# Optimization experiments

Measured on AMD Instinct MI355X. Metric: run time of the kernel, lower is better.

Reference implementation:

```python
import jax, jax.numpy as jnp
import numpy as np

N_QUAT = 4
VERONESE_DIM = 10
OUT_FEATURES = 132

# static index sets matching torch.triu_indices(4, 4)
_rows, _cols = np.triu_indices(N_QUAT)          # 10 upper-tri entries
_mask = _rows != _cols
TRIU_ROWS = jnp.asarray(_rows)
TRIU_COLS = jnp.asarray(_cols)
SYM_ROWS = jnp.asarray(_cols[_mask])            # mirrored lower-tri
SYM_COLS = jnp.asarray(_rows[_mask])
SYM_Z_IDX = jnp.asarray(np.nonzero(_mask)[0])


def setup_inputs() -> dict:
    key = jax.random.key(0)
    k_z, k_w1, k_w2 = jax.random.split(key, 3)
    B, D_IN, D_HID, D_OUT_NN = 65536, 256, 1024, 128
    z = jax.random.normal(k_z, (B, D_IN), dtype=jnp.float32)
    W1 = jax.random.normal(k_w1, (D_IN, D_HID), dtype=jnp.float32) * 0.02
    b1 = jnp.zeros((D_HID,), dtype=jnp.float32)
    W2 = jax.random.normal(k_w2, (D_HID, D_OUT_NN), dtype=jnp.float32) * 0.02
    b2 = jnp.zeros((D_OUT_NN,), dtype=jnp.float32)
    return {"z": z, "W1": W1, "b1": b1, "W2": W2, "b2": b2}


def _recover_quat(z_v):
    # z_v: (B, 10) -> symmetric (B, 4, 4) -> top eigenvector -> (B, 4)
    B = z_v.shape[0]
    M = jnp.zeros((B, N_QUAT, N_QUAT), dtype=z_v.dtype)
    M = M.at[:, TRIU_ROWS, TRIU_COLS].set(z_v)
    M = M.at[:, SYM_ROWS, SYM_COLS].set(z_v[:, SYM_Z_IDX])
    _, vecs = jnp.linalg.eigh(M)          # eigenvalues ascending
    q = vecs[:, :, -1]                    # eigenvector of largest eigenvalue
    sign = jnp.sign(q[:, 0:1] + 1e-9)
    return q * sign


def reference(z, W1, b1, W2, b2):
    orig_shape = z.shape
    zf = z.reshape(-1, orig_shape[-1])           # (B, in_features)
    q_pred = _recover_quat(zf[:, :VERONESE_DIM])  # (B, 4)
    h = jax.nn.relu(zf @ W1 + b1)
    others = h @ W2 + b2                          # (B, 128)
    B = zf.shape[0]
    out = jnp.zeros((B, OUT_FEATURES), dtype=zf.dtype)
    out = out.at[:, :N_QUAT].set(q_pred)          # quat_indices = [0,1,2,3]
    out = out.at[:, N_QUAT:].set(others)          # non_quat = [4..131]
    return out.reshape(*orig_shape[:-1], OUT_FEATURES)
```

## Files before the change

kernel.cpp:

```cpp
#include <hip/hip_runtime.h>


typedef short s16x8 __attribute__((ext_vector_type(8)));
typedef float f32x4 __attribute__((ext_vector_type(4)));
typedef float f32x16 __attribute__((ext_vector_type(16)));
typedef unsigned char u8;

__device__ __forceinline__ f32x16 mfma32(s16x8 a, s16x8 b, f32x16 c) {
    return __builtin_amdgcn_mfma_f32_32x32x16_bf16(a, b, c, 0, 0, 0);
}

__device__ __forceinline__ short f2bf(float f) {
    unsigned int u = __float_as_uint(f);
    u = (u + 0x7fffu + ((u >> 16) & 1u)) >> 16;
    return (short)u;
}

__device__ __forceinline__ unsigned cvt_pk(float lo, float hi) {
    unsigned r;
    asm("v_cvt_pk_bf16_f32 %0, %1, %2" : "=v"(r) : "v"(lo), "v"(hi));
    return r;
}

__device__ __forceinline__ void pl32swap(unsigned& a, unsigned& b) {
    asm("v_permlane32_swap_b32 %0, %1" : "+v"(a), "+v"(b));
}

__device__ __forceinline__ void gload_lds16(const void* g, void* l) {
    __builtin_amdgcn_global_load_lds(
        (const __attribute__((address_space(1))) unsigned int*)g,
        (__attribute__((address_space(3))) unsigned int*)l, 16, 0, 0);
}

__global__ __launch_bounds__(256) void prep_weights(
    const float* __restrict__ W1, const float* __restrict__ W2,
    uint4* __restrict__ w1t, uint4* __restrict__ w2t)
{
    int tid = blockIdx.x * 256 + threadIdx.x;
    int hl = (tid >> 5) & 1, r32 = tid & 31;
    union { short b[8]; uint4 v; } pk;
    if (tid < 32768) {
        int s  = (tid >> 6) & 15;
        int ct = (tid >> 10) & 1;
        int c  = tid >> 11;
        int k0 = s * 16 + hl * 8;
        int n1 = c * 64 + ct * 32 + r32;
        #pragma unroll
        for (int j = 0; j < 8; ++j)
            pk.b[j] = f2bf(W1[(k0 + j) * 1024 + n1]);
        w1t[tid] = pk.v;
    } else {
        int g  = tid - 32768;
        int nt = (g >> 6) & 3;
        int K  = g >> 8;
        int k0 = K * 16 + hl * 8;
        int n2 = nt * 32 + r32;
        #pragma unroll
        for (int j = 0; j < 8; ++j)
            pk.b[j] = f2bf(W2[(k0 + j) * 128 + n2]);
        w2t[g] = pk.v;
    }
}

__global__ __launch_bounds__(256, 2) void fused_all(
    const float* __restrict__ z, const float* __restrict__ b1,
    const float* __restrict__ b2, const uint4* __restrict__ w1t,
    const uint4* __restrict__ w2t, float* __restrict__ out)
{
    __shared__ __align__(16) u8 lds[69632];

    const int t    = threadIdx.x;
    const int lane = t & 63;
    const int w    = t >> 6;
    const int hl   = lane >> 5;
    const int r32  = lane & 31;
    const int bm0  = blockIdx.x * 128;
    const int rowbase = bm0 + w * 32;

    #pragma unroll
    for (int i = 0; i < 8; ++i) {
        int f = i * 256 + t;
        gload_lds16(w1t + f, lds + f * 16);
    }
    gload_lds16(b1 + t * 4, lds + 65536 + t * 16);

    if (lane < 32) {
        int row = rowbase + lane;
        const float* zr = z + (size_t)row * 256;
        float4 v0 = *(const float4*)(zr);
        float4 v1 = *(const float4*)(zr + 4);
        float2 v2 = *(const float2*)(zr + 8);

        float A[4][4] = {{v0.x, v0.y, v0.z, v0.w},
                         {v0.y, v1.x, v1.y, v1.z},
                         {v0.z, v1.y, v1.w, v2.x},
                         {v0.w, v1.z, v2.x, v2.y}};
        float V[4][4] = {{1.f, 0.f, 0.f, 0.f},
                         {0.f, 1.f, 0.f, 0.f},
                         {0.f, 0.f, 1.f, 0.f},
                         {0.f, 0.f, 0.f, 1.f}};

#define ROT(p, qq) do {                                                   \
        float apq  = A[p][qq];                                            \
        float tau  = (A[qq][qq] - A[p][p]) *                              \
                     __builtin_amdgcn_rcpf(2.0f * apq);                   \
        float tt   = __builtin_amdgcn_rcpf(                               \
                        fabsf(tau) +                                      \
                        __builtin_amdgcn_sqrtf(fmaf(tau, tau, 1.0f)));    \
        tt = copysignf(tt, tau);                                          \
        tt = (fabsf(apq) > 1e-20f) ? tt : 0.0f;                           \
        float cth = __builtin_amdgcn_rsqf(fmaf(tt, tt, 1.0f));            \
        float sth = tt * cth;                                             \
        _Pragma("unroll")                                                 \
        for (int k = 0; k < 4; ++k) {                                     \
            float akp = A[k][p], akq = A[k][qq];                          \
            A[k][p]  = cth * akp - sth * akq;                             \
            A[k][qq] = sth * akp + cth * akq;                             \
        }                                                                 \
        _Pragma("unroll")                                                 \
        for (int k = 0; k < 4; ++k) {                                     \
            float apk = A[p][k], aqk = A[qq][k];                          \
            A[p][k]  = cth * apk - sth * aqk;                             \
            A[qq][k] = sth * apk + cth * aqk;                             \
        }                                                                 \
        _Pragma("unroll")                                                 \
        for (int k = 0; k < 4; ++k) {                                     \
            float vkp = V[k][p], vkq = V[k][qq];                          \
            V[k][p]  = cth * vkp - sth * vkq;                             \
            V[k][qq] = sth * vkp + cth * vkq;                             \
        }                                                                 \
    } while (0)

        #pragma unroll 1
        for (int sweep = 0; sweep < 6; ++sweep) {
            ROT(0, 1); ROT(0, 2); ROT(0, 3); ROT(1, 2); ROT(1, 3); ROT(2, 3);
        }
#undef ROT

        float bv = A[0][0];
        float q0 = V[0][0], q1 = V[1][0], q2 = V[2][0], q3 = V[3][0];
        #pragma unroll
        for (int k = 1; k < 4; ++k) {
            bool better = A[k][k] > bv;
            bv = better ? A[k][k] : bv;
            q0 = better ? V[0][k] : q0;
            q1 = better ? V[1][k] : q1;
            q2 = better ? V[2][k] : q2;
            q3 = better ? V[3][k] : q3;
        }
        float sgn = (q0 + 1e-9f) >= 0.0f ? 1.0f : -1.0f;
        *(float4*)(out + (size_t)row * 132) =
            make_float4(sgn * q0, sgn * q1, sgn * q2, sgn * q3);
    }

    s16x8 zf[16];
    {
        const float* zp = z + (size_t)(rowbase + r32) * 256 + hl * 8;
        #pragma unroll
        for (int s = 0; s < 16; ++s) {
            float4 a0 = *(const float4*)(zp + s * 16);
            float4 a1 = *(const float4*)(zp + s * 16 + 4);
            union { unsigned u[4]; s16x8 v; } pk;
            pk.u[0] = cvt_pk(a0.x, a0.y);
            pk.u[1] = cvt_pk(a0.z, a0.w);
            pk.u[2] = cvt_pk(a1.x, a1.y);
            pk.u[3] = cvt_pk(a1.z, a1.w);
            zf[s] = pk.v;
        }
    }

    const f32x16 zero16 = {0.f,0.f,0.f,0.f, 0.f,0.f,0.f,0.f,
                           0.f,0.f,0.f,0.f, 0.f,0.f,0.f,0.f};
    f32x16 acc2[4];
    #pragma unroll
    for (int nt = 0; nt < 4; ++nt) acc2[nt] = zero16;

    __syncthreads();

    const u8* const aW0  = lds + lane * 16;
    const u8* const aW1  = lds + 32768 + lane * 16;
    const u8* const blsp = lds + 65536 + hl * 16;
    const s16x8* const w2b = (const s16x8*)w2t + lane;

    u8* const s1b0 = lds;
    u8* const s1b1 = lds + 32768;

    auto chunk = [&](int c, const u8* a, u8* s1dst) {
        const s16x8* w2c = w2b + c * 1024;
        s16x8 w2f[4][4];
        #pragma unroll
        for (int ks = 0; ks < 2; ++ks)
            #pragma unroll
            for (int nt = 0; nt < 4; ++nt)
                w2f[ks][nt] = w2c[(ks * 4 + nt) * 64];

        if (c < 15) {
            const uint4* s1 = w1t + (c + 1) * 2048;
            #pragma unroll
            for (int i = 0; i < 8; ++i) {
                int f = i * 256 + t;
                gload_lds16(s1 + f, s1dst + f * 16);
            }
        }

        const u8* bb = blsp + c * 256;
        s16x8 hf[4];

        auto tile = [&](int ct) {
            __builtin_amdgcn_s_setprio(1);
            f32x16 d = zero16;
            #pragma unroll
            for (int s = 0; s < 16; ++s) {
                s16x8 afr = *(const s16x8*)(a + (ct * 16 + s) * 1024);
                d = mfma32(afr, zf[s], d);
            }
            __builtin_amdgcn_s_setprio(0);
            unsigned Plo[4], Phi[4];
            #pragma unroll
            for (int g = 0; g < 4; ++g) {
                f32x4 bv = *(const f32x4*)(bb + ct * 128 + g * 32);
                Plo[g] = cvt_pk(fmaxf(d[4*g+0] + bv[0], 0.f),
                                fmaxf(d[4*g+1] + bv[1], 0.f));
                Phi[g] = cvt_pk(fmaxf(d[4*g+2] + bv[2], 0.f),
                                fmaxf(d[4*g+3] + bv[3], 0.f));
            }
            #pragma unroll
            for (int f = 0; f < 2; ++f) {
                unsigned a0 = Plo[2*f], b0 = Plo[2*f+1];
                unsigned a1 = Phi[2*f], b1 = Phi[2*f+1];
                pl32swap(a0, b0);
                pl32swap(a1, b1);
                union { unsigned u[4]; s16x8 v; } fr;
                fr.u[0] = a0; fr.u[1] = a1; fr.u[2] = b0; fr.u[3] = b1;
                hf[ct * 2 + f] = fr.v;
            }
        };

        tile(0);
        #pragma unroll
        for (int ks = 2; ks < 4; ++ks)
            #pragma unroll
            for (int nt = 0; nt < 4; ++nt)
                w2f[ks][nt] = w2c[(ks * 4 + nt) * 64];
        __builtin_amdgcn_s_setprio(1);
        #pragma unroll
        for (int ks = 0; ks < 2; ++ks)
            #pragma unroll
            for (int nt = 0; nt < 4; ++nt)
                acc2[nt] = mfma32(hf[ks], w2f[ks][nt], acc2[nt]);
        __builtin_amdgcn_s_setprio(0);

        tile(1);
        __builtin_amdgcn_s_setprio(1);
        #pragma unroll
        for (int ks = 2; ks < 4; ++ks)
            #pragma unroll
            for (int nt = 0; nt < 4; ++nt)
                acc2[nt] = mfma32(hf[ks], w2f[ks][nt], acc2[nt]);
        __builtin_amdgcn_s_setprio(0);

        __syncthreads();
    };

    #pragma unroll 1
    for (int cc = 0; cc < 8; ++cc) {
        chunk(2 * cc,     aW0, s1b1);
        chunk(2 * cc + 1, aW1, s1b0);
    }

    #pragma unroll
    for (int nt = 0; nt < 4; ++nt) {
        const float b2v = b2[nt * 32 + r32];
        #pragma unroll
        for (int r = 0; r < 16; ++r) {
            int m = w * 32 + (r & 3) + 8 * (r >> 2) + 4 * hl;
            out[(size_t)(bm0 + m) * 132 + 4 + nt * 32 + r32] =
                acc2[nt][r] + b2v;
        }
    }
}

extern "C" void kernel_launch(void* const* d_in, const int* in_sizes, int n_in,
                              void* d_out, int out_size, void* d_ws, size_t ws_size,
                              hipStream_t stream) {
    const float* z  = (const float*)d_in[0];
    const float* W1 = (const float*)d_in[1];
    const float* b1 = (const float*)d_in[2];
    const float* W2 = (const float*)d_in[3];
    const float* b2 = (const float*)d_in[4];
    float* out = (float*)d_out;

    uint4* w1t = (uint4*)d_ws;
    uint4* w2t = (uint4*)((char*)d_ws + 512 * 1024);

    hipLaunchKernelGGL(prep_weights, dim3(192), dim3(256), 0, stream,
                       W1, W2, w1t, w2t);
    hipLaunchKernelGGL(fused_all, dim3(512), dim3(256), 0, stream,
                       z, b1, b2, (const uint4*)w1t, (const uint4*)w2t, out);
}
```

Before: 73.13 us.

## Software-pipeline GEMM2 of previous chunk into GEMM1 MFMA loop

Restructures the fused MLP chunk loop so the second GEMM for chunk c-1 runs interleaved with the first GEMM of chunk c. The two 32-wide GEMM1 tiles are computed together, and the bias/ReLU/bf16 packing is deferred to the end of the chunk. A prologue chunk and an epilogue GEMM2 are added. The aim is to hide the dependency stall between GEMM1 output and GEMM2 input, at the cost of more live registers (hfp, two accumulators).

```diff
diff --git a/kernel.cpp b/kernel.cpp
--- a/kernel.cpp
+++ b/kernel.cpp
@@ -185,14 +185,40 @@
     u8* const s1b0 = lds;
     u8* const s1b1 = lds + 32768;
 
-    auto chunk = [&](int c, const u8* a, u8* s1dst) {
-        const s16x8* w2c = w2b + c * 1024;
+    s16x8 hfp[4];
+
+    auto pack = [&](const f32x16& d, const u8* bb, int ct, s16x8* hfo) {
+        unsigned Plo[4], Phi[4];
+        #pragma unroll
+        for (int g = 0; g < 4; ++g) {
+            f32x4 bv = *(const f32x4*)(bb + ct * 128 + g * 32);
+            Plo[g] = cvt_pk(fmaxf(d[4*g+0] + bv[0], 0.f),
+                            fmaxf(d[4*g+1] + bv[1], 0.f));
+            Phi[g] = cvt_pk(fmaxf(d[4*g+2] + bv[2], 0.f),
+                            fmaxf(d[4*g+3] + bv[3], 0.f));
+        }
+        #pragma unroll
+        for (int f = 0; f < 2; ++f) {
+            unsigned a0 = Plo[2*f], b0 = Plo[2*f+1];
+            unsigned a1 = Phi[2*f], b1 = Phi[2*f+1];
+            pl32swap(a0, b0);
+            pl32swap(a1, b1);
+            union { unsigned u[4]; s16x8 v; } fr;
+            fr.u[0] = a0; fr.u[1] = a1; fr.u[2] = b0; fr.u[3] = b1;
+            hfo[f] = fr.v;
+        }
+    };
+
+    auto chunk = [&](int c, const u8* a, u8* s1dst, bool DO_G2) {
         s16x8 w2f[4][4];
-        #pragma unroll
-        for (int ks = 0; ks < 2; ++ks)
+        const s16x8* w2c = w2b + (c - 1) * 1024;
+        if (DO_G2) {
             #pragma unroll
-            for (int nt = 0; nt < 4; ++nt)
-                w2f[ks][nt] = w2c[(ks * 4 + nt) * 64];
+            for (int ks = 0; ks < 2; ++ks)
+                #pragma unroll
+                for (int nt = 0; nt < 4; ++nt)
+                    w2f[ks][nt] = w2c[(ks * 4 + nt) * 64];
+        }
 
         if (c < 15) {
             const uint4* s1 = w1t + (c + 1) * 2048;
@@ -204,68 +230,54 @@
         }
 
         const u8* bb = blsp + c * 256;
-        s16x8 hf[4];
-
-        auto tile = [&](int ct) {
-            __builtin_amdgcn_s_setprio(1);
-            f32x16 d = zero16;
-            #pragma unroll
-            for (int s = 0; s < 16; ++s) {
-                s16x8 afr = *(const s16x8*)(a + (ct * 16 + s) * 1024);
-                d = mfma32(afr, zf[s], d);
+
+        __builtin_amdgcn_s_setprio(1);
+        f32x16 d0 = zero16, d1 = zero16;
+        #pragma unroll
+        for (int s = 0; s < 16; ++s) {
+            s16x8 a0 = *(const s16x8*)(a + s * 1024);
+            s16x8 a1 = *(const s16x8*)(a + (16 + s) * 1024);
+            d0 = mfma32(a0, zf[s], d0);
+            d1 = mfma32(a1, zf[s], d1);
+            if (DO_G2 && s == 4) {
+                #pragma unroll
+                for (int ks = 2; ks < 4; ++ks)
+                    #pragma unroll
+                    for (int nt = 0; nt < 4; ++nt)
+                        w2f[ks][nt] = w2c[(ks * 4 + nt) * 64];
             }
-            __builtin_amdgcn_s_setprio(0);
-            unsigned Plo[4], Phi[4];
-            #pragma unroll
-            for (int g = 0; g < 4; ++g) {
-                f32x4 bv = *(const f32x4*)(bb + ct * 128 + g * 32);
-                Plo[g] = cvt_pk(fmaxf(d[4*g+0] + bv[0], 0.f),
-                                fmaxf(d[4*g+1] + bv[1], 0.f));
-                Phi[g] = cvt_pk(fmaxf(d[4*g+2] + bv[2], 0.f),
-                                fmaxf(d[4*g+3] + bv[3], 0.f));
+            if (DO_G2 && s >= 8) {
+                int i = s - 8, ks = i >> 1, nt0 = (i & 1) * 2;
+                acc2[nt0]     = mfma32(hfp[ks], w2f[ks][nt0],     acc2[nt0]);
+                acc2[nt0 + 1] = mfma32(hfp[ks], w2f[ks][nt0 + 1], acc2[nt0 + 1]);
             }
-            #pragma unroll
-            for (int f = 0; f < 2; ++f) {
-                unsigned a0 = Plo[2*f], b0 = Plo[2*f+1];
-                unsigned a1 = Phi[2*f], b1 = Phi[2*f+1];
-                pl32swap(a0, b0);
-                pl32swap(a1, b1);
-                union { unsigned u[4]; s16x8 v; } fr;
-                fr.u[0] = a0; fr.u[1] = a1; fr.u[2] = b0; fr.u[3] = b1;
-                hf[ct * 2 + f] = fr.v;
-            }
-        };
-
-        tile(0);
-        #pragma unroll
-        for (int ks = 2; ks < 4; ++ks)
-            #pragma unroll
-            for (int nt = 0; nt < 4; ++nt)
-                w2f[ks][nt] = w2c[(ks * 4 + nt) * 64];
-        __builtin_amdgcn_s_setprio(1);
-        #pragma unroll
-        for (int ks = 0; ks < 2; ++ks)
-            #pragma unroll
-            for (int nt = 0; nt < 4; ++nt)
-                acc2[nt] = mfma32(hf[ks], w2f[ks][nt], acc2[nt]);
+        }
         __builtin_amdgcn_s_setprio(0);
 
-        tile(1);
-        __builtin_amdgcn_s_setprio(1);
-        #pragma unroll
-        for (int ks = 2; ks < 4; ++ks)
-            #pragma unroll
-            for (int nt = 0; nt < 4; ++nt)
-                acc2[nt] = mfma32(hf[ks], w2f[ks][nt], acc2[nt]);
-        __builtin_amdgcn_s_setprio(0);
+        pack(d0, bb, 0, hfp);
+        pack(d1, bb, 1, hfp + 2);
 
         __syncthreads();
     };
 
+    chunk(0, aW0, s1b1, false);
     #pragma unroll 1
-    for (int cc = 0; cc < 8; ++cc) {
-        chunk(2 * cc,     aW0, s1b1);
-        chunk(2 * cc + 1, aW1, s1b0);
+    for (int cc = 0; cc < 7; ++cc) {
+        chunk(2 * cc + 1, aW1, s1b0, true);
+        chunk(2 * cc + 2, aW0, s1b1, true);
+    }
+    chunk(15, aW1, s1b0, true);
+
+    {
+        const s16x8* w2c = w2b + 15 * 1024;
+        #pragma unroll
+        for (int ks = 0; ks < 4; ++ks) {
+            #pragma unroll
+            for (int nt = 0; nt < 4; ++nt) {
+                s16x8 bfr = w2c[(ks * 4 + nt) * 64];
+                acc2[nt] = mfma32(hfp[ks], bfr, acc2[nt]);
+            }
+        }
     }
 
     #pragma unroll
```

After: 76.25 us. +4.3%, slower.

## Drop LDS staging of W1; single-wave blocks read weights directly from global

Applied to the files above, without the earlier changes.

Replaces the 4-wave block that cooperatively double-buffers W1 chunks and b1 in LDS with 1-wave blocks (2048 of them). Each wave now loads its W1 fragments, b1 and W2 directly from global memory via L2/cache. This removes the LDS staging, the barriers and the 68KB LDS footprint that limited occupancy. In exchange every wave fetches the full weight matrix itself, which raises global/L2 traffic fourfold and puts load latency directly in front of the MFMAs.

```diff
diff --git a/kernel.cpp b/kernel.cpp
--- a/kernel.cpp
+++ b/kernel.cpp
@@ -24,12 +24,6 @@
 
 __device__ __forceinline__ void pl32swap(unsigned& a, unsigned& b) {
     asm("v_permlane32_swap_b32 %0, %1" : "+v"(a), "+v"(b));
-}
-
-__device__ __forceinline__ void gload_lds16(const void* g, void* l) {
-    __builtin_amdgcn_global_load_lds(
-        (const __attribute__((address_space(1))) unsigned int*)g,
-        (__attribute__((address_space(3))) unsigned int*)l, 16, 0, 0);
 }
 
 __global__ __launch_bounds__(256) void prep_weights(
@@ -62,27 +56,15 @@
     }
 }
 
-__global__ __launch_bounds__(256, 2) void fused_all(
+__global__ __launch_bounds__(64, 2) void fused_all(
     const float* __restrict__ z, const float* __restrict__ b1,
     const float* __restrict__ b2, const uint4* __restrict__ w1t,
     const uint4* __restrict__ w2t, float* __restrict__ out)
 {
-    __shared__ __align__(16) u8 lds[69632];
-
-    const int t    = threadIdx.x;
-    const int lane = t & 63;
-    const int w    = t >> 6;
+    const int lane = threadIdx.x & 63;
     const int hl   = lane >> 5;
     const int r32  = lane & 31;
-    const int bm0  = blockIdx.x * 128;
-    const int rowbase = bm0 + w * 32;
-
-    #pragma unroll
-    for (int i = 0; i < 8; ++i) {
-        int f = i * 256 + t;
-        gload_lds16(w1t + f, lds + f * 16);
-    }
-    gload_lds16(b1 + t * 4, lds + 65536 + t * 16);
+    const int rowbase = blockIdx.x * 32;
 
     if (lane < 32) {
         int row = rowbase + lane;
@@ -175,97 +157,55 @@
     #pragma unroll
     for (int nt = 0; nt < 4; ++nt) acc2[nt] = zero16;
 
-    __syncthreads();
-
-    const u8* const aW0  = lds + lane * 16;
-    const u8* const aW1  = lds + 32768 + lane * 16;
-    const u8* const blsp = lds + 65536 + hl * 16;
+    const s16x8* const w1b = (const s16x8*)w1t + lane;
     const s16x8* const w2b = (const s16x8*)w2t + lane;
-
-    u8* const s1b0 = lds;
-    u8* const s1b1 = lds + 32768;
-
-    auto chunk = [&](int c, const u8* a, u8* s1dst) {
+    const float* const bbp = b1 + hl * 4;
+
+    s16x8 hf[4];
+
+    auto pack = [&](const f32x16& d, int c, int ct, s16x8* hfo) {
+        unsigned Plo[4], Phi[4];
+        #pragma unroll
+        for (int g = 0; g < 4; ++g) {
+            f32x4 bv = *(const f32x4*)(bbp + c * 64 + ct * 32 + g * 8);
+            Plo[g] = cvt_pk(fmaxf(d[4*g+0] + bv[0], 0.f),
+                            fmaxf(d[4*g+1] + bv[1], 0.f));
+            Phi[g] = cvt_pk(fmaxf(d[4*g+2] + bv[2], 0.f),
+                            fmaxf(d[4*g+3] + bv[3], 0.f));
+        }
+        #pragma unroll
+        for (int f = 0; f < 2; ++f) {
+            unsigned a0 = Plo[2*f], b0 = Plo[2*f+1];
+            unsigned a1 = Phi[2*f], b1_ = Phi[2*f+1];
+            pl32swap(a0, b0);
+            pl32swap(a1, b1_);
+            union { unsigned u[4]; s16x8 v; } fr;
+            fr.u[0] = a0; fr.u[1] = a1; fr.u[2] = b0; fr.u[3] = b1_;
+            hfo[f] = fr.v;
+        }
+    };
+
+    #pragma unroll 2
+    for (int c = 0; c < 16; ++c) {
+        const s16x8* w1c = w1b + c * 2048;
+        #pragma unroll
+        for (int ct = 0; ct < 2; ++ct) {
+            f32x16 d = zero16;
+            __builtin_amdgcn_s_setprio(1);
+            #pragma unroll
+            for (int s = 0; s < 16; ++s)
+                d = mfma32(w1c[(ct * 16 + s) * 64], zf[s], d);
+            __builtin_amdgcn_s_setprio(0);
+            pack(d, c, ct, hf + 2 * ct);
+        }
         const s16x8* w2c = w2b + c * 1024;
-        s16x8 w2f[4][4];
-        #pragma unroll
-        for (int ks = 0; ks < 2; ++ks)
+        __builtin_amdgcn_s_setprio(1);
+        #pragma unroll
+        for (int ks = 0; ks < 4; ++ks)
             #pragma unroll
             for (int nt = 0; nt < 4; ++nt)
-                w2f[ks][nt] = w2c[(ks * 4 + nt) * 64];
-
-        if (c < 15) {
-            const uint4* s1 = w1t + (c + 1) * 2048;
-            #pragma unroll
-            for (int i = 0; i < 8; ++i) {
-                int f = i * 256 + t;
-                gload_lds16(s1 + f, s1dst + f * 16);
-            }
-        }
-
-        const u8* bb = blsp + c * 256;
-        s16x8 hf[4];
-
-        auto tile = [&](int ct) {
-            __builtin_amdgcn_s_setprio(1);
-            f32x16 d = zero16;
-            #pragma unroll
-            for (int s = 0; s < 16; ++s) {
-                s16x8 afr = *(const s16x8*)(a + (ct * 16 + s) * 1024);
-                d = mfma32(afr, zf[s], d);
-            }
-            __builtin_amdgcn_s_setprio(0);
-            unsigned Plo[4], Phi[4];
-            #pragma unroll
-            for (int g = 0; g < 4; ++g) {
-                f32x4 bv = *(const f32x4*)(bb + ct * 128 + g * 32);
-                Plo[g] = cvt_pk(fmaxf(d[4*g+0] + bv[0], 0.f),
-                                fmaxf(d[4*g+1] + bv[1], 0.f));
-                Phi[g] = cvt_pk(fmaxf(d[4*g+2] + bv[2], 0.f),
-                                fmaxf(d[4*g+3] + bv[3], 0.f));
-            }
-            #pragma unroll
-            for (int f = 0; f < 2; ++f) {
-                unsigned a0 = Plo[2*f], b0 = Plo[2*f+1];
-                unsigned a1 = Phi[2*f], b1 = Phi[2*f+1];
-                pl32swap(a0, b0);
-                pl32swap(a1, b1);
-                union { unsigned u[4]; s16x8 v; } fr;
-                fr.u[0] = a0; fr.u[1] = a1; fr.u[2] = b0; fr.u[3] = b1;
-                hf[ct * 2 + f] = fr.v;
-            }
-        };
-
-        tile(0);
-        #pragma unroll
-        for (int ks = 2; ks < 4; ++ks)
-            #pragma unroll
-            for (int nt = 0; nt < 4; ++nt)
-                w2f[ks][nt] = w2c[(ks * 4 + nt) * 64];
-        __builtin_amdgcn_s_setprio(1);
-        #pragma unroll
-        for (int ks = 0; ks < 2; ++ks)
-            #pragma unroll
-            for (int nt = 0; nt < 4; ++nt)
-                acc2[nt] = mfma32(hf[ks], w2f[ks][nt], acc2[nt]);
+                acc2[nt] = mfma32(hf[ks], w2c[(ks * 4 + nt) * 64], acc2[nt]);
         __builtin_amdgcn_s_setprio(0);
-
-        tile(1);
-        __builtin_amdgcn_s_setprio(1);
-        #pragma unroll
-        for (int ks = 2; ks < 4; ++ks)
-            #pragma unroll
-            for (int nt = 0; nt < 4; ++nt)
-                acc2[nt] = mfma32(hf[ks], w2f[ks][nt], acc2[nt]);
-        __builtin_amdgcn_s_setprio(0);
-
-        __syncthreads();
-    };
-
-    #pragma unroll 1
-    for (int cc = 0; cc < 8; ++cc) {
-        chunk(2 * cc,     aW0, s1b1);
-        chunk(2 * cc + 1, aW1, s1b0);
     }
 
     #pragma unroll
@@ -273,8 +213,8 @@
         const float b2v = b2[nt * 32 + r32];
         #pragma unroll
         for (int r = 0; r < 16; ++r) {
-            int m = w * 32 + (r & 3) + 8 * (r >> 2) + 4 * hl;
-            out[(size_t)(bm0 + m) * 132 + 4 + nt * 32 + r32] =
+            int m = (r & 3) + 8 * (r >> 2) + 4 * hl;
+            out[(size_t)(rowbase + m) * 132 + 4 + nt * 32 + r32] =
                 acc2[nt][r] + b2v;
         }
     }
@@ -295,6 +235,6 @@
 
     hipLaunchKernelGGL(prep_weights, dim3(192), dim3(256), 0, stream,
                        W1, W2, w1t, w2t);
-    hipLaunchKernelGGL(fused_all, dim3(512), dim3(256), 0, stream,
+    hipLaunchKernelGGL(fused_all, dim3(2048), dim3(64), 0, stream,
                        z, b1, b2, (const uint4*)w1t, (const uint4*)w2t, out);
 }
```

After: 148.2 us. 2.03x slower.

## Restructure chunk pipeline with partial vmcnt waits and interleaved dual-tile MFMA

Applied to the files above, without the earlier changes.

Replaces the trailing __syncthreads per chunk with a leading s_barrier preceded by a partial s_waitcnt vmcnt(16), so the W2 register prefetches stay in flight across the barrier while the LDS-targeted W1 loads are complete. Peels the first and last chunks so the next-chunk W1 prefetch is skipped statically. Computes both GEMM1 tiles in one interleaved loop (two independent accumulators) to raise MFMA ILP, then packs and runs all GEMM2 MFMAs together. This raises register pressure and relies on the vmcnt ordering assumption being correct for the LDS async loads.

```diff
diff --git a/kernel.cpp b/kernel.cpp
--- a/kernel.cpp
+++ b/kernel.cpp
@@ -185,16 +185,35 @@
     u8* const s1b0 = lds;
     u8* const s1b1 = lds + 32768;
 
-    auto chunk = [&](int c, const u8* a, u8* s1dst) {
-        const s16x8* w2c = w2b + c * 1024;
-        s16x8 w2f[4][4];
-        #pragma unroll
-        for (int ks = 0; ks < 2; ++ks)
-            #pragma unroll
-            for (int nt = 0; nt < 4; ++nt)
-                w2f[ks][nt] = w2c[(ks * 4 + nt) * 64];
-
-        if (c < 15) {
+    auto pack = [&](const f32x16& d, const u8* bb, int ct, s16x8* hfo) {
+        unsigned Plo[4], Phi[4];
+        #pragma unroll
+        for (int g = 0; g < 4; ++g) {
+            f32x4 bv = *(const f32x4*)(bb + ct * 128 + g * 32);
+            Plo[g] = cvt_pk(fmaxf(d[4*g+0] + bv[0], 0.f),
+                            fmaxf(d[4*g+1] + bv[1], 0.f));
+            Phi[g] = cvt_pk(fmaxf(d[4*g+2] + bv[2], 0.f),
+                            fmaxf(d[4*g+3] + bv[3], 0.f));
+        }
+        #pragma unroll
+        for (int f = 0; f < 2; ++f) {
+            unsigned a0 = Plo[2*f], b0 = Plo[2*f+1];
+            unsigned a1 = Phi[2*f], b1_ = Phi[2*f+1];
+            pl32swap(a0, b0);
+            pl32swap(a1, b1_);
+            union { unsigned u[4]; s16x8 v; } fr;
+            fr.u[0] = a0; fr.u[1] = a1; fr.u[2] = b0; fr.u[3] = b1_;
+            hfo[f] = fr.v;
+        }
+    };
+
+    auto chunk = [&](int c, const u8* a, u8* s1dst, bool FIRST, bool LAST) {
+        if (!FIRST) {
+            asm volatile("s_waitcnt vmcnt(16)" ::: "memory");
+        }
+        __builtin_amdgcn_s_barrier();
+
+        if (!LAST) {
             const uint4* s1 = w1t + (c + 1) * 2048;
             #pragma unroll
             for (int i = 0; i < 8; ++i) {
@@ -203,78 +222,55 @@
             }
         }
 
-        const u8* bb = blsp + c * 256;
-        s16x8 hf[4];
-
-        auto tile = [&](int ct) {
-            __builtin_amdgcn_s_setprio(1);
-            f32x16 d = zero16;
-            #pragma unroll
-            for (int s = 0; s < 16; ++s) {
-                s16x8 afr = *(const s16x8*)(a + (ct * 16 + s) * 1024);
-                d = mfma32(afr, zf[s], d);
-            }
-            __builtin_amdgcn_s_setprio(0);
-            unsigned Plo[4], Phi[4];
-            #pragma unroll
-            for (int g = 0; g < 4; ++g) {
-                f32x4 bv = *(const f32x4*)(bb + ct * 128 + g * 32);
-                Plo[g] = cvt_pk(fmaxf(d[4*g+0] + bv[0], 0.f),
-                                fmaxf(d[4*g+1] + bv[1], 0.f));
-                Phi[g] = cvt_pk(fmaxf(d[4*g+2] + bv[2], 0.f),
-                                fmaxf(d[4*g+3] + bv[3], 0.f));
-            }
-            #pragma unroll
-            for (int f = 0; f < 2; ++f) {
-                unsigned a0 = Plo[2*f], b0 = Plo[2*f+1];
-                unsigned a1 = Phi[2*f], b1 = Phi[2*f+1];
-                pl32swap(a0, b0);
-                pl32swap(a1, b1);
-                union { unsigned u[4]; s16x8 v; } fr;
-                fr.u[0] = a0; fr.u[1] = a1; fr.u[2] = b0; fr.u[3] = b1;
-                hf[ct * 2 + f] = fr.v;
-            }
-        };
-
-        tile(0);
-        #pragma unroll
-        for (int ks = 2; ks < 4; ++ks)
+        const s16x8* w2c = w2b + c * 1024;
+        s16x8 w2f[4][4];
+        #pragma unroll
+        for (int ks = 0; ks < 4; ++ks)
             #pragma unroll
             for (int nt = 0; nt < 4; ++nt)
                 w2f[ks][nt] = w2c[(ks * 4 + nt) * 64];
+
+        const u8* bb = blsp + c * 256;
+        s16x8 hf[4];
+
         __builtin_amdgcn_s_setprio(1);
-        #pragma unroll
-        for (int ks = 0; ks < 2; ++ks)
+        f32x16 d0 = zero16, d1 = zero16;
+        #pragma unroll
+        for (int s = 0; s < 16; ++s) {
+            s16x8 a0 = *(const s16x8*)(a + s * 1024);
+            s16x8 a1 = *(const s16x8*)(a + (16 + s) * 1024);
+            d0 = mfma32(a0, zf[s], d0);
+            d1 = mfma32(a1, zf[s], d1);
+        }
+        __builtin_amdgcn_s_setprio(0);
+
+        pack(d0, bb, 0, hf);
+        pack(d1, bb, 1, hf + 2);
+
+        __builtin_amdgcn_s_setprio(1);
+        #pragma unroll
+        for (int ks = 0; ks < 4; ++ks)
             #pragma unroll
             for (int nt = 0; nt < 4; ++nt)
                 acc2[nt] = mfma32(hf[ks], w2f[ks][nt], acc2[nt]);
         __builtin_amdgcn_s_setprio(0);
-
-        tile(1);
-        __builtin_amdgcn_s_setprio(1);
-        #pragma unroll
-        for (int ks = 2; ks < 4; ++ks)
-            #pragma unroll
-            for (int nt = 0; nt < 4; ++nt)
-                acc2[nt] = mfma32(hf[ks], w2f[ks][nt], acc2[nt]);
-        __builtin_amdgcn_s_setprio(0);
-
-        __syncthreads();
     };
 
+    chunk(0, aW0, s1b1, true, false);
     #pragma unroll 1
-    for (int cc = 0; cc < 8; ++cc) {
-        chunk(2 * cc,     aW0, s1b1);
-        chunk(2 * cc + 1, aW1, s1b0);
-    }
+    for (int cc = 0; cc < 7; ++cc) {
+        chunk(2 * cc + 1, aW1, s1b0, false, false);
+        chunk(2 * cc + 2, aW0, s1b1, false, false);
+    }
+    chunk(15, aW1, s1b0, false, true);
 
     #pragma unroll
     for (int nt = 0; nt < 4; ++nt) {
         const float b2v = b2[nt * 32 + r32];
         #pragma unroll
         for (int r = 0; r < 16; ++r) {
-            int m = w * 32 + (r & 3) + 8 * (r >> 2) + 4 * hl;
-            out[(size_t)(bm0 + m) * 132 + 4 + nt * 32 + r32] =
+            int m = (r & 3) + 8 * (r >> 2) + 4 * hl;
+            out[(size_t)(bm0 + w * 32 + m) * 132 + 4 + nt * 32 + r32] =
                 acc2[nt][r] + b2v;
         }
     }
```

Measured after the change: 75.01 us. +2.6%, slower.
